# Kernel optimization log

Measured on AMD Instinct MI355X. Metric: run time of the kernel, lower is better.

The kernel has to match this reference:

```python
import jax, jax.numpy as jnp
import numpy as np
import math

D_MODEL = 1024
N_HEADS = 16
BATCH = 2
SEQ = 2048

def setup_inputs() -> dict:
    key = jax.random.key(0)
    ks = jax.random.split(key, 5)
    d = D_MODEL
    lim_qkv = 1.0 / math.sqrt(d)
    x = jax.random.normal(ks[0], (BATCH, SEQ, d), dtype=jnp.float32)
    qkv_w = jax.random.uniform(ks[1], (3 * d, d), dtype=jnp.float32, minval=-lim_qkv, maxval=lim_qkv)
    qkv_b = jax.random.uniform(ks[2], (3 * d,), dtype=jnp.float32, minval=-lim_qkv, maxval=lim_qkv)
    out_w = jax.random.uniform(ks[3], (d, d), dtype=jnp.float32, minval=-lim_qkv, maxval=lim_qkv)
    out_b = jax.random.uniform(ks[4], (d,), dtype=jnp.float32, minval=-lim_qkv, maxval=lim_qkv)
    return {"x": x, "qkv_w": qkv_w, "qkv_b": qkv_b, "out_w": out_w, "out_b": out_b}

def reference(x, qkv_w, qkv_b, out_w, out_b):
    b, s, d = x.shape
    h = N_HEADS
    hd = d // h
    # note: original uses float division for scale: sqrt(in_features / n_heads)
    scale = math.sqrt(d / h)
    qkv = x @ qkv_w.T + qkv_b                      # [b, s, 3d]
    q, k, v = jnp.split(qkv, 3, axis=-1)           # each [b, s, d]
    def heads(t):
        return t.reshape(b, s, h, hd).transpose(0, 2, 1, 3)  # [b, h, s, hd]
    qh, kh, vh = heads(q), heads(k), heads(v)
    # faithful quirk: scores = k @ q^T (k as query, q as key)
    scores = jnp.einsum('bhid,bhjd->bhij', kh, qh) / scale   # [b, h, s, s]
    alpha = jax.nn.softmax(scores, axis=-1)
    attn = jnp.einsum('bhij,bhjd->bhid', alpha, vh)          # [b, h, s, hd]
    attn = attn.transpose(0, 2, 1, 3).reshape(b, s, d)       # [b, s, d]
    return attn @ out_w.T + out_b
```

## Files before the change

kernel.cpp:

```cpp
#include <hip/hip_runtime.h>
#include <hip/hip_fp16.h>

#define D_MODEL 1024
#define N_HEADS 16
#define HEAD_DIM 64
#define BATCH 2
#define SEQ 2048
#define ROWS (BATCH*SEQ)

#define K_SCALE 0.18033688011112042f

using h8v = __attribute__((ext_vector_type(8))) _Float16;
using h4v = __attribute__((ext_vector_type(4))) _Float16;
using g2v = __attribute__((ext_vector_type(2))) __fp16;
using g4v = __attribute__((ext_vector_type(4))) __fp16;
using us8 = __attribute__((ext_vector_type(8))) unsigned short;
using f4v = __attribute__((ext_vector_type(4))) float;

__device__ __forceinline__ ushort f2h_u(float x) { return __half_as_ushort(__float2half(x)); }
__device__ __forceinline__ void splith(float x, ushort& h, ushort& l) {
    __half hh_ = __float2half(x);
    h = __half_as_ushort(hh_);
    l = f2h_u(x - __half2float(hh_));
}

__device__ __forceinline__ size_t fidx(int row, int k) {
    return ((size_t)((row >> 7) * 32 + (k >> 5)) << 12)
         + (size_t)(((row & 127) >> 4) << 9)
         + (size_t)(((row & 15) * 4 + ((k & 31) >> 3)) << 3) + (k & 7);
}

__device__ __forceinline__ void async_lds16(const ushort* g, ushort* l) {
    __builtin_amdgcn_global_load_lds(
        (const __attribute__((address_space(1))) unsigned int*)g,
        (__attribute__((address_space(3))) unsigned int*)l, 16, 0, 0);
}

__global__ __launch_bounds__(256)
void prep_kernel(const float* __restrict__ x, const float* __restrict__ qw,
                 ushort* __restrict__ xh, ushort* __restrict__ qwh)
{
    const int b = blockIdx.x, t = threadIdx.x;
    if (b < 4096) {
        const int i = b * 256 + t;
        const int row = i >> 8, k4 = (i & 255) * 4;
        const float4 v = ((const float4*)x)[i];
        ushort4 h;
        h.x = f2h_u(v.x); h.y = f2h_u(v.y); h.z = f2h_u(v.z); h.w = f2h_u(v.w);
        *(ushort4*)&xh[fidx(row, k4)] = h;
    } else {
        const int i = (b - 4096) * 256 + t;
        const int row = i >> 8, k4 = (i & 255) * 4;
        const float4 v = ((const float4*)qw)[i];
        ushort4 h;
        h.x = f2h_u(v.x); h.y = f2h_u(v.y); h.z = f2h_u(v.z); h.w = f2h_u(v.w);
        *(ushort4*)&qwh[fidx(row, k4)] = h;
    }
}

__global__ __launch_bounds__(256, 5)
void gemm_qkv(const ushort* __restrict__ Af, const ushort* __restrict__ Wf,
              const float* __restrict__ bias,
              ushort* __restrict__ Qh, ushort* __restrict__ Kh,
              ushort* __restrict__ Vt,
              const float* __restrict__ ow,
              ushort* __restrict__ owh, ushort* __restrict__ owl)
{
    __shared__ ushort sA[2][4096], sW[2][2048];
    const int t = threadIdx.x;
    const int lin = blockIdx.x;

    if (lin >= 1536) {
        const int i = (lin - 1536) * 256 + t;
        const int row = i >> 8, k4 = (i & 255) * 4;
        const float4 v = ((const float4*)ow)[i];
        const size_t o = fidx(row, k4);
        ushort4 h, l;
        splith(v.x, h.x, l.x); splith(v.y, h.y, l.y);
        splith(v.z, h.z, l.z); splith(v.w, h.w, l.w);
        *(ushort4*)&owh[o] = h; *(ushort4*)&owl[o] = l;
        return;
    }

    const int lane = t & 63, wv = t >> 6;
    const int tx = lane & 15, g = lane >> 4;
    const int xcd = lin & 7, r = lin >> 3;
    const int mb = xcd * 4 + (r & 3);
    const int nb = r >> 2;
    const int at0 = (wv >> 1) * 4, wt0 = (wv & 1) * 2;
    const int fo = (tx * 4 + g) * 8;
    const size_t wbase = ((size_t)(nb & 1)) << 11;

    f4v acc[8];
#pragma unroll
    for (int i = 0; i < 8; i++)
#pragma unroll
        for (int e = 0; e < 4; e++) acc[i][e] = 0.f;

    {
        const size_t ao = ((size_t)(mb * 32)) << 12;
        const size_t wo = (((size_t)((nb >> 1) * 32)) << 12) + wbase;
#pragma unroll
        for (int c = 0; c < 2; c++) {
            const int o = (t + c * 256) * 8;
            async_lds16(Af + ao + o, &sA[0][o]);
        }
        async_lds16(Wf + wo + t * 8, &sW[0][t * 8]);
    }

    for (int kt = 0; kt < 32; kt++) {
        const int p = kt & 1;
        __syncthreads();
        if (kt < 31) {
            const size_t ao = ((size_t)(mb * 32 + kt + 1)) << 12;
            const size_t wo = (((size_t)((nb >> 1) * 32 + kt + 1)) << 12) + wbase;
#pragma unroll
            for (int c = 0; c < 2; c++) {
                const int o = (t + c * 256) * 8;
                async_lds16(Af + ao + o, &sA[p ^ 1][o]);
            }
            async_lds16(Wf + wo + t * 8, &sW[p ^ 1][t * 8]);
        }
        h8v ah[4], wh[2];
#pragma unroll
        for (int i = 0; i < 4; i++)
            ah[i] = *(const h8v*)&sA[p][(at0 + i) * 512 + fo];
#pragma unroll
        for (int i = 0; i < 2; i++)
            wh[i] = *(const h8v*)&sW[p][(wt0 + i) * 512 + fo];
        if (nb < 32) {
#pragma unroll
            for (int wi = 0; wi < 2; wi++)
#pragma unroll
                for (int ai = 0; ai < 4; ai++)
                    acc[wi * 4 + ai] = __builtin_amdgcn_mfma_f32_16x16x32_f16(wh[wi], ah[ai], acc[wi * 4 + ai], 0, 0, 0);
        } else {
#pragma unroll
            for (int ai = 0; ai < 4; ai++)
#pragma unroll
                for (int wi = 0; wi < 2; wi++)
                    acc[ai * 2 + wi] = __builtin_amdgcn_mfma_f32_16x16x32_f16(ah[ai], wh[wi], acc[ai * 2 + wi], 0, 0, 0);
        }
    }

    if (nb < 32) {
        const int part = nb >> 4;
        ushort* dst = part ? Kh : Qh;
        const float scale = part ? K_SCALE : 1.0f;
#pragma unroll
        for (int wi = 0; wi < 2; wi++) {
            const int gf0 = nb * 64 + (wv & 1) * 32 + wi * 16 + g * 4;
            const float4 bv = *(const float4*)&bias[gf0];
            const int gfl = gf0 & 1023;
            const int hh = gfl >> 6;
            const int dd = gfl & 63;
#pragma unroll
            for (int ai = 0; ai < 4; ai++) {
                const int s = mb * 128 + (wv >> 1) * 64 + ai * 16 + tx;
                const int bb = s >> 11, srel = s & 2047;
                const size_t idx = (size_t)(bb * N_HEADS + hh) * 131072
                    + (size_t)(srel >> 4) * 1024 + (size_t)(dd >> 5) * 512
                    + ((srel & 15) * 4 + ((dd & 31) >> 3)) * 8 + (dd & 7);
                const f4v a = acc[wi * 4 + ai];
                ushort4 h4;
                h4.x = f2h_u((a[0] + bv.x) * scale);
                h4.y = f2h_u((a[1] + bv.y) * scale);
                h4.z = f2h_u((a[2] + bv.z) * scale);
                h4.w = f2h_u((a[3] + bv.w) * scale);
                *(ushort4*)&dst[idx] = h4;
            }
        }
    } else {
#pragma unroll
        for (int wi = 0; wi < 2; wi++) {
            const int gf = nb * 64 + (wv & 1) * 32 + wi * 16 + tx;
            const float bv = bias[gf];
            const int gfl = gf & 1023;
            const int hh = gfl >> 6;
            const int dl = gfl & 63;
            const int t0 = mb * 2 + (wv >> 1);
            const int bb = t0 >> 5;
            const size_t base = (size_t)(bb * N_HEADS + hh) * 131072
                + (size_t)(t0 & 31) * 4096
                + (size_t)((dl >> 4) & 3) * 512
                + (size_t)g * 128 + (size_t)(dl & 15) * 8;
#pragma unroll
            for (int aip = 0; aip < 2; aip++) {
                const f4v a0 = acc[(2 * aip) * 2 + wi];
                const f4v a1 = acc[(2 * aip + 1) * 2 + wi];
                us8 s;
                s[0] = f2h_u(a0[0] + bv); s[1] = f2h_u(a0[1] + bv);
                s[2] = f2h_u(a0[2] + bv); s[3] = f2h_u(a0[3] + bv);
                s[4] = f2h_u(a1[0] + bv); s[5] = f2h_u(a1[1] + bv);
                s[6] = f2h_u(a1[2] + bv); s[7] = f2h_u(a1[3] + bv);
                *(us8*)&Vt[base + (size_t)aip * 2048] = s;
            }
        }
    }
}

__global__ __launch_bounds__(256)
void attn_mfma(const ushort* __restrict__ Kf, const ushort* __restrict__ Qf,
               const ushort* __restrict__ Vf,
               ushort* __restrict__ Oh, ushort* __restrict__ Ol)
{
    __shared__ ushort lds[32768];
    ushort* KR = lds;
    ushort* bufs = lds + 8192;

    const int t = threadIdx.x, lane = t & 63, wv = t >> 6;
    const int tx = lane & 15, g = lane >> 4;
    const int lin = blockIdx.x;
    const int xcd = lin & 7, ix = lin >> 3;
    const int bh = xcd * 4 + (ix >> 4);
    const int it = ix & 15;
    const int b = bh >> 4, h = bh & 15;
    const int i0 = it * 128;
    const size_t hb = (size_t)bh * 131072;

    {
        const size_t kb = hb + (size_t)it * 8192;
#pragma unroll
        for (int c = 0; c < 4; c++) {
            const int o = (t + c * 256) * 8;
            async_lds16(Kf + kb + o, KR + o);
        }
#pragma unroll
        for (int c = 0; c < 2; c++) {
            const int o = (t + c * 256) * 8;
            async_lds16(Qf + hb + o, bufs + o);
            async_lds16(Vf + hb + o, bufs + 4096 + o);
        }
    }
    __syncthreads();

    const int fo = (tx * 4 + g) * 8;
    const int vo = (g * 16 + tx) * 8;
    h8v kf[2][2];
#pragma unroll
    for (int is = 0; is < 2; is++)
#pragma unroll
        for (int kk = 0; kk < 2; kk++)
            kf[is][kk] = *(const h8v*)&KR[((wv * 2 + is) * 2 + kk) * 512 + fo];

    {
        const size_t off = hb + 4096;
#pragma unroll
        for (int c = 0; c < 2; c++) {
            const int o = (t + c * 256) * 8;
            async_lds16(Qf + off + o, bufs + 8192 + o);
            async_lds16(Vf + off + o, bufs + 8192 + 4096 + o);
        }
    }

    f4v O[2][4];
    float l_acc[2] = {0.f, 0.f};
#pragma unroll
    for (int is = 0; is < 2; is++)
#pragma unroll
        for (int ht = 0; ht < 4; ht++)
#pragma unroll
            for (int e = 0; e < 4; e++) O[is][ht][e] = 0.f;

    h4v php[2][4];

    {
        const ushort* sQ = bufs;
        f4v sc[2][4];
#pragma unroll
        for (int is = 0; is < 2; is++)
#pragma unroll
            for (int jn = 0; jn < 4; jn++)
#pragma unroll
                for (int e = 0; e < 4; e++) sc[is][jn][e] = 0.f;
#pragma unroll
        for (int kk = 0; kk < 2; kk++)
#pragma unroll
            for (int jn = 0; jn < 4; jn++) {
                const h8v qf = *(const h8v*)&sQ[(jn * 2 + kk) * 512 + fo];
#pragma unroll
                for (int is = 0; is < 2; is++)
                    sc[is][jn] = __builtin_amdgcn_mfma_f32_16x16x32_f16(qf, kf[is][kk], sc[is][jn], 0, 0, 0);
            }
#pragma unroll
        for (int is = 0; is < 2; is++)
#pragma unroll
            for (int jn = 0; jn < 4; jn++) {
                const float p0 = __builtin_amdgcn_exp2f(sc[is][jn][0]);
                const float p1 = __builtin_amdgcn_exp2f(sc[is][jn][1]);
                const float p2 = __builtin_amdgcn_exp2f(sc[is][jn][2]);
                const float p3 = __builtin_amdgcn_exp2f(sc[is][jn][3]);
                l_acc[is] += (p0 + p1) + (p2 + p3);
                const g2v plo = __builtin_amdgcn_cvt_pkrtz(p0, p1);
                const g2v phi = __builtin_amdgcn_cvt_pkrtz(p2, p3);
                const g4v pk = __builtin_shufflevector(plo, phi, 0, 1, 2, 3);
                php[is][jn] = __builtin_bit_cast(h4v, pk);
            }
    }

    int bp = 0, bc = 1, bn = 2;
    for (int jt = 1; jt < SEQ / 64; jt++) {
        __syncthreads();
        if (jt < SEQ / 64 - 1) {
            const size_t off = hb + (size_t)(jt + 1) * 4096;
#pragma unroll
            for (int c = 0; c < 2; c++) {
                const int o = (t + c * 256) * 8;
                async_lds16(Qf + off + o, bufs + bn * 8192 + o);
                async_lds16(Vf + off + o, bufs + bn * 8192 + 4096 + o);
            }
        }
        const ushort* sQ = bufs + bc * 8192;
        const ushort* sVp = bufs + bp * 8192 + 4096;

        f4v sc[2][4];
#pragma unroll
        for (int is = 0; is < 2; is++)
#pragma unroll
            for (int jn = 0; jn < 4; jn++)
#pragma unroll
                for (int e = 0; e < 4; e++) sc[is][jn][e] = 0.f;
#pragma unroll
        for (int kk = 0; kk < 2; kk++)
#pragma unroll
            for (int jn = 0; jn < 4; jn++) {
                const h8v qf = *(const h8v*)&sQ[(jn * 2 + kk) * 512 + fo];
#pragma unroll
                for (int is = 0; is < 2; is++)
                    sc[is][jn] = __builtin_amdgcn_mfma_f32_16x16x32_f16(qf, kf[is][kk], sc[is][jn], 0, 0, 0);
            }

#pragma unroll
        for (int jc = 0; jc < 2; jc++) {
            h8v p8[2];
#pragma unroll
            for (int is = 0; is < 2; is++)
                p8[is] = __builtin_shufflevector(php[is][jc * 2], php[is][jc * 2 + 1],
                                                 0, 1, 2, 3, 4, 5, 6, 7);
#pragma unroll
            for (int ht = 0; ht < 4; ht++) {
                const h8v vf = *(const h8v*)&sVp[jc * 2048 + ht * 512 + vo];
#pragma unroll
                for (int is = 0; is < 2; is++)
                    O[is][ht] = __builtin_amdgcn_mfma_f32_16x16x32_f16(vf, p8[is], O[is][ht], 0, 0, 0);
            }
        }

#pragma unroll
        for (int is = 0; is < 2; is++)
#pragma unroll
            for (int jn = 0; jn < 4; jn++) {
                const float p0 = __builtin_amdgcn_exp2f(sc[is][jn][0]);
                const float p1 = __builtin_amdgcn_exp2f(sc[is][jn][1]);
                const float p2 = __builtin_amdgcn_exp2f(sc[is][jn][2]);
                const float p3 = __builtin_amdgcn_exp2f(sc[is][jn][3]);
                l_acc[is] += (p0 + p1) + (p2 + p3);
                const g2v plo = __builtin_amdgcn_cvt_pkrtz(p0, p1);
                const g2v phi = __builtin_amdgcn_cvt_pkrtz(p2, p3);
                const g4v pk = __builtin_shufflevector(plo, phi, 0, 1, 2, 3);
                php[is][jn] = __builtin_bit_cast(h4v, pk);
            }

        const int tmp = bp; bp = bc; bc = bn; bn = tmp;
    }

    {
        const ushort* sVp = bufs + bp * 8192 + 4096;
#pragma unroll
        for (int jc = 0; jc < 2; jc++) {
            h8v p8[2];
#pragma unroll
            for (int is = 0; is < 2; is++)
                p8[is] = __builtin_shufflevector(php[is][jc * 2], php[is][jc * 2 + 1],
                                                 0, 1, 2, 3, 4, 5, 6, 7);
#pragma unroll
            for (int ht = 0; ht < 4; ht++) {
                const h8v vf = *(const h8v*)&sVp[jc * 2048 + ht * 512 + vo];
#pragma unroll
                for (int is = 0; is < 2; is++)
                    O[is][ht] = __builtin_amdgcn_mfma_f32_16x16x32_f16(vf, p8[is], O[is][ht], 0, 0, 0);
            }
        }
    }

#pragma unroll
    for (int is = 0; is < 2; is++) {
        float l = l_acc[is];
        l += __shfl_xor(l, 16);
        l += __shfl_xor(l, 32);
        const float inv = 1.0f / l;
        const int row = b * SEQ + i0 + (wv * 2 + is) * 16 + tx;
#pragma unroll
        for (int ht = 0; ht < 4; ht++) {
            const int k0 = h * 64 + ht * 16 + g * 4;
            const size_t o = fidx(row, k0);
            ushort4 hv, lv;
            float v;
            v = O[is][ht][0] * inv; splith(v, hv.x, lv.x);
            v = O[is][ht][1] * inv; splith(v, hv.y, lv.y);
            v = O[is][ht][2] * inv; splith(v, hv.z, lv.z);
            v = O[is][ht][3] * inv; splith(v, hv.w, lv.w);
            *(ushort4*)&Oh[o] = hv;
            *(ushort4*)&Ol[o] = lv;
        }
    }
}

__global__ __launch_bounds__(256, 4)
void gemm_out(const ushort* __restrict__ Af, const ushort* __restrict__ Alf,
              const ushort* __restrict__ Wf, const ushort* __restrict__ Wlf,
              const float* __restrict__ bias, float* __restrict__ out)
{
    __shared__ ushort sA[2][4096], sW[2][4096];
    const int t = threadIdx.x, lane = t & 63, wv = t >> 6;
    const int tx = lane & 15, g = lane >> 4;
    const int lin = blockIdx.x;
    const int xcd = lin & 7, r = lin >> 3;
    const int nb = xcd * 2 + (r & 1);
    const int mb = r >> 1;
    const int at0 = (wv >> 1) * 2, wt0 = (wv & 1) * 2;
    const int fo = (tx * 4 + g) * 8;
    const size_t abase = ((size_t)(mb & 1)) << 11;
    const size_t wbase = ((size_t)(nb & 1)) << 11;

    f4v acc[4];
#pragma unroll
    for (int i = 0; i < 4; i++)
#pragma unroll
        for (int e = 0; e < 4; e++) acc[i][e] = 0.f;

    {
        const size_t ao = (((size_t)((mb >> 1) * 32)) << 12) + abase;
        const size_t wo = (((size_t)((nb >> 1) * 32)) << 12) + wbase;
        const int o = t * 8;
        async_lds16(Af + ao + o, &sA[0][o]);
        async_lds16(Alf + ao + o, &sA[0][2048 + o]);
        async_lds16(Wf + wo + o, &sW[0][o]);
        async_lds16(Wlf + wo + o, &sW[0][2048 + o]);
    }

    for (int kt = 0; kt < 32; kt++) {
        const int p = kt & 1;
        __syncthreads();
        if (kt < 31) {
            const size_t ao = (((size_t)((mb >> 1) * 32 + kt + 1)) << 12) + abase;
            const size_t wo = (((size_t)((nb >> 1) * 32 + kt + 1)) << 12) + wbase;
            const int o = t * 8;
            async_lds16(Af + ao + o, &sA[p ^ 1][o]);
            async_lds16(Alf + ao + o, &sA[p ^ 1][2048 + o]);
            async_lds16(Wf + wo + o, &sW[p ^ 1][o]);
            async_lds16(Wlf + wo + o, &sW[p ^ 1][2048 + o]);
        }
        h8v ah[2], al[2], wh[2], wl[2];
#pragma unroll
        for (int i = 0; i < 2; i++) {
            ah[i] = *(const h8v*)&sA[p][(at0 + i) * 512 + fo];
            al[i] = *(const h8v*)&sA[p][2048 + (at0 + i) * 512 + fo];
            wh[i] = *(const h8v*)&sW[p][(wt0 + i) * 512 + fo];
            wl[i] = *(const h8v*)&sW[p][2048 + (wt0 + i) * 512 + fo];
        }
#pragma unroll
        for (int wi = 0; wi < 2; wi++)
#pragma unroll
            for (int ai = 0; ai < 2; ai++) {
                acc[wi * 2 + ai] = __builtin_amdgcn_mfma_f32_16x16x32_f16(wh[wi], ah[ai], acc[wi * 2 + ai], 0, 0, 0);
                acc[wi * 2 + ai] = __builtin_amdgcn_mfma_f32_16x16x32_f16(wh[wi], al[ai], acc[wi * 2 + ai], 0, 0, 0);
                acc[wi * 2 + ai] = __builtin_amdgcn_mfma_f32_16x16x32_f16(wl[wi], ah[ai], acc[wi * 2 + ai], 0, 0, 0);
            }
    }

#pragma unroll
    for (int wi = 0; wi < 2; wi++) {
        const int gf0 = nb * 64 + (wv & 1) * 32 + wi * 16 + g * 4;
        const float4 bv = *(const float4*)&bias[gf0];
#pragma unroll
        for (int ai = 0; ai < 2; ai++) {
            const int tok = mb * 64 + (wv >> 1) * 32 + ai * 16 + tx;
            const f4v a = acc[wi * 2 + ai];
            float4 o;
            o.x = a[0] + bv.x;
            o.y = a[1] + bv.y;
            o.z = a[2] + bv.z;
            o.w = a[3] + bv.w;
            *(float4*)&out[(size_t)tok * D_MODEL + gf0] = o;
        }
    }
}

extern "C" void kernel_launch(void* const* d_in, const int* in_sizes, int n_in,
                              void* d_out, int out_size, void* d_ws, size_t ws_size,
                              hipStream_t stream) {
    const float* x     = (const float*)d_in[0];
    const float* qkv_w = (const float*)d_in[1];
    const float* qkv_b = (const float*)d_in[2];
    const float* out_w = (const float*)d_in[3];
    const float* out_b = (const float*)d_in[4];
    float* out = (float*)d_out;

    const size_t FB = (size_t)ROWS * D_MODEL;
    const size_t MM = (size_t)D_MODEL * D_MODEL;
    ushort* u   = (ushort*)d_ws;
    ushort* xh  = u;
    ushort* Ol  = u + FB;
    ushort* Qh  = u + 2 * FB;
    ushort* Kh  = u + 3 * FB;
    ushort* Vt  = u + 4 * FB;
    ushort* qwh = u + 5 * FB;
    ushort* owh = u + 5 * FB + 3 * MM;
    ushort* owl = owh + MM;

    prep_kernel<<<7168, 256, 0, stream>>>(x, qkv_w, xh, qwh);
    gemm_qkv<<<2560, 256, 0, stream>>>(xh, qwh, qkv_b, Qh, Kh, Vt, out_w, owh, owl);
    attn_mfma<<<512, 256, 0, stream>>>(Kh, Qh, Vt, xh, Ol);
    gemm_out<<<1024, 256, 0, stream>>>(xh, Ol, owh, owl, out_b, out);
}
```

Baseline: 200.9 us.

## Process two KV tiles per barrier using a five-slot LDS ring buffer

```diff
diff --git a/kernel.cpp b/kernel.cpp
--- a/kernel.cpp
+++ b/kernel.cpp
@@ -204,9 +204,7 @@
                const ushort* __restrict__ Vf,
                ushort* __restrict__ Oh, ushort* __restrict__ Ol)
 {
-    __shared__ ushort lds[32768];
-    ushort* KR = lds;
-    ushort* bufs = lds + 8192;
+    __shared__ ushort lds[40960];
 
     const int t = threadIdx.x, lane = t & 63, wv = t >> 6;
     const int tx = lane & 15, g = lane >> 4;
@@ -218,40 +216,41 @@
     const int i0 = it * 128;
     const size_t hb = (size_t)bh * 131072;
 
+    const int fo = (tx * 4 + g) * 8;
+    const int vo = (g * 16 + tx) * 8;
+
+    auto dmaQV = [&](int jt, int k) {
+        const size_t off = hb + (size_t)jt * 4096;
+        ushort* d = lds + k * 8192;
+#pragma unroll
+        for (int c = 0; c < 2; c++) {
+            const int o = (t + c * 256) * 8;
+            async_lds16(Qf + off + o, d + o);
+            async_lds16(Vf + off + o, d + 4096 + o);
+        }
+    };
+
     {
         const size_t kb = hb + (size_t)it * 8192;
+        ushort* KR = lds + 3 * 8192;
 #pragma unroll
         for (int c = 0; c < 4; c++) {
             const int o = (t + c * 256) * 8;
             async_lds16(Kf + kb + o, KR + o);
         }
-#pragma unroll
-        for (int c = 0; c < 2; c++) {
-            const int o = (t + c * 256) * 8;
-            async_lds16(Qf + hb + o, bufs + o);
-            async_lds16(Vf + hb + o, bufs + 4096 + o);
-        }
+        dmaQV(0, 0);
     }
     __syncthreads();
 
-    const int fo = (tx * 4 + g) * 8;
-    const int vo = (g * 16 + tx) * 8;
     h8v kf[2][2];
 #pragma unroll
     for (int is = 0; is < 2; is++)
 #pragma unroll
         for (int kk = 0; kk < 2; kk++)
-            kf[is][kk] = *(const h8v*)&KR[((wv * 2 + is) * 2 + kk) * 512 + fo];
-
-    {
-        const size_t off = hb + 4096;
-#pragma unroll
-        for (int c = 0; c < 2; c++) {
-            const int o = (t + c * 256) * 8;
-            async_lds16(Qf + off + o, bufs + 8192 + o);
-            async_lds16(Vf + off + o, bufs + 8192 + 4096 + o);
-        }
-    }
+            kf[is][kk] = *(const h8v*)&lds[3 * 8192 + ((wv * 2 + is) * 2 + kk) * 512 + fo];
+
+    dmaQV(1, 1);
+    dmaQV(2, 2);
 
     f4v O[2][4];
     float l_acc[2] = {0.f, 0.f};
@@ -264,8 +263,7 @@
 
     h4v php[2][4];
 
-    {
-        const ushort* sQ = bufs;
+    auto step = [&](const ushort* sQ, const ushort* sVp) {
         f4v sc[2][4];
 #pragma unroll
         for (int is = 0; is < 2; is++)
@@ -282,6 +280,23 @@
                 for (int is = 0; is < 2; is++)
                     sc[is][jn] = __builtin_amdgcn_mfma_f32_16x16x32_f16(qf, kf[is][kk], sc[is][jn], 0, 0, 0);
             }
+
+#pragma unroll
+        for (int jc = 0; jc < 2; jc++) {
+            h8v p8[2];
+#pragma unroll
+            for (int is = 0; is < 2; is++)
+                p8[is] = __builtin_shufflevector(php[is][jc * 2], php[is][jc * 2 + 1],
+                                                 0, 1, 2, 3, 4, 5, 6, 7);
+#pragma unroll
+            for (int ht = 0; ht < 4; ht++) {
+                const h8v vf = *(const h8v*)&sVp[jc * 2048 + ht * 512 + vo];
+#pragma unroll
+                for (int is = 0; is < 2; is++)
+                    O[is][ht] = __builtin_amdgcn_mfma_f32_16x16x32_f16(vf, p8[is], O[is][ht], 0, 0, 0);
+            }
+        }
+
 #pragma unroll
         for (int is = 0; is < 2; is++)
 #pragma unroll
@@ -296,23 +311,10 @@
                 const g4v pk = __builtin_shufflevector(plo, phi, 0, 1, 2, 3);
                 php[is][jn] = __builtin_bit_cast(h4v, pk);
             }
-    }
-
-    int bp = 0, bc = 1, bn = 2;
-    for (int jt = 1; jt < SEQ / 64; jt++) {
-        __syncthreads();
-        if (jt < SEQ / 64 - 1) {
-            const size_t off = hb + (size_t)(jt + 1) * 4096;
-#pragma unroll
-            for (int c = 0; c < 2; c++) {
-                const int o = (t + c * 256) * 8;
-                async_lds16(Qf + off + o, bufs + bn * 8192 + o);
-                async_lds16(Vf + off + o, bufs + bn * 8192 + 4096 + o);
-            }
-        }
-        const ushort* sQ = bufs + bc * 8192;
-        const ushort* sVp = bufs + bp * 8192 + 4096;
-
+    };
+
+    {
+        const ushort* sQ = lds;
         f4v sc[2][4];
 #pragma unroll
         for (int is = 0; is < 2; is++)
@@ -329,23 +331,6 @@
                 for (int is = 0; is < 2; is++)
                     sc[is][jn] = __builtin_amdgcn_mfma_f32_16x16x32_f16(qf, kf[is][kk], sc[is][jn], 0, 0, 0);
             }
-
-#pragma unroll
-        for (int jc = 0; jc < 2; jc++) {
-            h8v p8[2];
-#pragma unroll
-            for (int is = 0; is < 2; is++)
-                p8[is] = __builtin_shufflevector(php[is][jc * 2], php[is][jc * 2 + 1],
-                                                 0, 1, 2, 3, 4, 5, 6, 7);
-#pragma unroll
-            for (int ht = 0; ht < 4; ht++) {
-                const h8v vf = *(const h8v*)&sVp[jc * 2048 + ht * 512 + vo];
-#pragma unroll
-                for (int is = 0; is < 2; is++)
-                    O[is][ht] = __builtin_amdgcn_mfma_f32_16x16x32_f16(vf, p8[is], O[is][ht], 0, 0, 0);
-            }
-        }
-
 #pragma unroll
         for (int is = 0; is < 2; is++)
 #pragma unroll
@@ -360,12 +345,27 @@
                 const g4v pk = __builtin_shufflevector(plo, phi, 0, 1, 2, 3);
                 php[is][jn] = __builtin_bit_cast(h4v, pk);
             }
-
-        const int tmp = bp; bp = bc; bc = bn; bn = tmp;
-    }
+    }
+
+    int a = 1, pv = 0;
+    for (int p = 0; p < 15; p++) {
+        __syncthreads();
+        const int a2 = (a + 1 == 5) ? 0 : a + 1;
+        const int d1 = (a2 + 1 == 5) ? 0 : a2 + 1;
+        const int d2 = (d1 + 1 == 5) ? 0 : d1 + 1;
+        const int j1 = 2 * p + 1;
+        dmaQV(j1 + 2, d1);
+        if (p < 14) dmaQV(j1 + 3, d2);
+        step(lds + a * 8192, lds + pv * 8192 + 4096);
+        step(lds + a2 * 8192, lds + a * 8192 + 4096);
+        pv = a2; a = d1;
+    }
+
+    __syncthreads();
+    step(lds + a * 8192, lds + pv * 8192 + 4096);
 
     {
-        const ushort* sVp = bufs + bp * 8192 + 4096;
+        const ushort* sVp = lds + a * 8192 + 4096;
 #pragma unroll
         for (int jc = 0; jc < 2; jc++) {
             h8v p8[2];
```

Result: no change. 204.7 us (+1.9%).
